# Optimization experiments

Hardware: AMD Instinct MI355X
Metric: run time of the kernel (lower is better)

The kernel has to match this reference:

```python
import jax, jax.numpy as jnp
import numpy as np

EMBED_DIM = 1024
NUM_HEADS = 16
HEAD_DIM = EMBED_DIM // NUM_HEADS


def setup_inputs() -> dict:
    key = jax.random.key(0)
    ks = jax.random.split(key, 5)
    B, N = 4, 2048
    s_in = 1.0 / np.sqrt(EMBED_DIM)
    return {
        "x": jax.random.normal(ks[0], (B, N, EMBED_DIM), dtype=jnp.float32),
        "qkv_w": jax.random.uniform(ks[1], (3 * EMBED_DIM, EMBED_DIM), jnp.float32, -s_in, s_in),
        "qkv_b": jax.random.uniform(ks[2], (3 * EMBED_DIM,), jnp.float32, -s_in, s_in),
        "o_w": jax.random.uniform(ks[3], (EMBED_DIM, EMBED_DIM), jnp.float32, -s_in, s_in),
        "o_b": jax.random.uniform(ks[4], (EMBED_DIM,), jnp.float32, -s_in, s_in),
    }


def reference(x, qkv_w, qkv_b, o_w, o_b):
    B, N, E = x.shape
    H, D = NUM_HEADS, HEAD_DIM
    # qkv: [B, N, 3E] -> [B, N, H, 3D] -> [B, H, N, 3D], then chunk last dim
    qkv = (jnp.einsum('bne,fe->bnf', x, qkv_w) + qkv_b)
    qkv = qkv.reshape(B, N, H, 3 * D).transpose(0, 2, 1, 3)
    q, k, v = jnp.split(qkv, 3, axis=-1)
    scale = 1.0 / np.sqrt(D)
    scores = jnp.einsum('bhqd,bhkd->bhqk', q, k) * scale
    attn = jax.nn.softmax(scores, axis=-1)  # dropout is identity in eval mode
    out = jnp.einsum('bhqk,bhkd->bhqd', attn, v)
    out = out.transpose(0, 2, 1, 3).reshape(B, N, E)
    return jnp.einsum('bne,fe->bnf', out, o_w) + o_b
```

## Files before the change

kernel.cpp:

```cpp
#include <hip/hip_runtime.h>

typedef unsigned short u16;
typedef float f32x4 __attribute__((ext_vector_type(4)));
typedef float f32x16 __attribute__((ext_vector_type(16)));
typedef short bf16x8 __attribute__((ext_vector_type(8)));
typedef int i32x2 __attribute__((ext_vector_type(2)));

__device__ __forceinline__ u16 f2bf(float f){
  union { float f; unsigned u; } x; x.f = f;
  unsigned r = (x.u + 0x7FFFu + ((x.u >> 16) & 1u)) >> 16;
  return (u16)r;
}

__device__ __forceinline__ unsigned cvtpk(float lo, float hi){
  unsigned r;
  asm("v_cvt_pk_bf16_f32 %0, %1, %2" : "=v"(r) : "v"(lo), "v"(hi));
  return r;
}

__device__ __forceinline__ f32x4 mfma_bf16(bf16x8 a, bf16x8 b, f32x4 c){
  return __builtin_amdgcn_mfma_f32_16x16x32_bf16(a, b, c, 0, 0, 0);
}

__device__ __forceinline__ f32x16 mfma32(bf16x8 a, bf16x8 b, f32x16 c){
  return __builtin_amdgcn_mfma_f32_32x32x16_bf16(a, b, c, 0, 0, 0);
}

__device__ __forceinline__ void gload16(const u16* g, u16* l){
  __builtin_amdgcn_global_load_lds((__attribute__((address_space(1))) void*)g,
                                   (__attribute__((address_space(3))) void*)l, 16, 0, 0);
}

__global__ void cvt_bf16(const float* __restrict__ in, u16* __restrict__ out, int n4){
  int stride = gridDim.x * blockDim.x;
  for (int i = blockIdx.x*blockDim.x + threadIdx.x; i < n4; i += stride){
    float4 v = ((const float4*)in)[i];
    ushort4 o;
    o.x = f2bf(v.x); o.y = f2bf(v.y); o.z = f2bf(v.z); o.w = f2bf(v.w);
    ((ushort4*)out)[i] = o;
  }
}

__device__ __forceinline__ void stage128x32(const u16* src, int ld, u16* lds, int tid){
  int wave = tid >> 6, lane = tid & 63;
#pragma unroll
  for (int i = 0; i < 2; i++){
    int chunk = i*256 + wave*64 + lane;
    int row = chunk >> 2, slot = chunk & 3;
    int col = ((slot ^ (row & 3)) << 3);
    gload16(src + (size_t)row*ld + col, lds + ((size_t)(i*256 + wave*64) << 3));
  }
}

template<int MODE>
__launch_bounds__(256)
__global__ void gemm_bt(const u16* __restrict__ A, const u16* __restrict__ Bw,
                        const float* __restrict__ bias,
                        u16* __restrict__ Qp, u16* __restrict__ Kp, u16* __restrict__ Vt,
                        float* __restrict__ Co, int M, int Nf, int K)
{
  __shared__ u16 lsA[2][128*32];
  __shared__ u16 lsB[2][128*32];
  int tid = threadIdx.x;
  int wave = tid >> 6, lane = tid & 63, grp = lane >> 4, l16 = lane & 15;
  int ntn = Nf >> 7;
  int bm = blockIdx.x / ntn, bn = blockIdx.x % ntn;
  const u16* Ab = A + (size_t)bm*128*K;
  const u16* Bb = Bw + (size_t)bn*128*K;
  int wm = wave >> 1, wn = wave & 1;
  f32x4 acc[4][4] = {};

  stage128x32(Ab, K, lsA[0], tid);
  stage128x32(Bb, K, lsB[0], tid);
  int nk = K >> 5;
  for (int t = 0; t < nk; t++){
    __syncthreads();
    int cur = t & 1;
    if (t + 1 < nk){
      stage128x32(Ab + ((t+1) << 5), K, lsA[cur^1], tid);
      stage128x32(Bb + ((t+1) << 5), K, lsB[cur^1], tid);
    }
    const u16* la = lsA[cur];
    const u16* lb = lsB[cur];
    bf16x8 af[4], bfr[4];
#pragma unroll
    for (int mf = 0; mf < 4; mf++){
      int row = wm*64 + mf*16 + l16;
      af[mf] = *(const bf16x8*)(la + row*32 + ((grp ^ (row & 3)) << 3));
    }
#pragma unroll
    for (int nf = 0; nf < 4; nf++){
      int row = wn*64 + nf*16 + l16;
      bfr[nf] = *(const bf16x8*)(lb + row*32 + ((grp ^ (row & 3)) << 3));
    }
#pragma unroll
    for (int mf = 0; mf < 4; mf++)
#pragma unroll
      for (int nf = 0; nf < 4; nf++)
        acc[mf][nf] = mfma_bf16(af[mf], bfr[nf], acc[mf][nf]);
  }

  int mrow0 = bm*128 + wm*64;
  int f0 = bn*128 + wn*64;
#pragma unroll
  for (int nf = 0; nf < 4; nf++){
    int f = f0 + nf*16 + l16;
    float bv = bias[f];
    if constexpr (MODE == 0){
      int h = f / 192, c = f % 192;
#pragma unroll
      for (int mf = 0; mf < 4; mf++){
        int mbase = mrow0 + mf*16 + grp*4;
        int bb = mbase >> 11, n0 = mbase & 2047;
        size_t bh = (size_t)bb*16 + h;
        if (c >= 128){
          ushort4 w;
          w.x = f2bf(acc[mf][nf][0] + bv);
          w.y = f2bf(acc[mf][nf][1] + bv);
          w.z = f2bf(acc[mf][nf][2] + bv);
          w.w = f2bf(acc[mf][nf][3] + bv);
          *(ushort4*)(Vt + (bh*64 + (size_t)(c - 128))*2048 + n0) = w;
        } else {
          u16* dst = (c < 64) ? Qp : Kp;
          float sc = (c < 64) ? 0.18033688011f : 1.0f;
          int cc = c & 63;
#pragma unroll
          for (int r = 0; r < 4; r++)
            dst[(bh*2048 + n0 + r)*64 + cc] = f2bf((acc[mf][nf][r] + bv) * sc);
        }
      }
    } else {
#pragma unroll
      for (int mf = 0; mf < 4; mf++){
        int mbase = mrow0 + mf*16 + grp*4;
#pragma unroll
        for (int r = 0; r < 4; r++)
          Co[(size_t)(mbase + r)*Nf + f] = acc[mf][nf][r] + bv;
      }
    }
  }
}

__device__ __forceinline__ void stage64x64(const u16* src, int ld, u16* lds, int tid){
  int wave = tid >> 6, lane = tid & 63;
#pragma unroll
  for (int i = 0; i < 2; i++){
    int chunk = i*256 + wave*64 + lane;
    int row = chunk >> 3, slot = chunk & 7;
    int col = ((slot ^ (row & 7)) << 3);
    gload16(src + (size_t)row*ld + col, lds + ((size_t)(i*256 + wave*64) << 3));
  }
}

__launch_bounds__(256, 4)
__global__ void attn_fwd(const u16* __restrict__ Qg, const u16* __restrict__ Kg,
                         const u16* __restrict__ Vtg, u16* __restrict__ Oa)
{
  __shared__ u16 kl[2][64*64];
  __shared__ u16 vl[2][64*64];
  int tid = threadIdx.x;
  int lane = tid & 63, wave = tid >> 6;
  int q32 = lane & 31, hi = lane >> 5;
  int bid = (blockIdx.x & 7) * 128 + (blockIdx.x >> 3);
  int bh = bid >> 4, qt = bid & 15;
  int b = bh >> 4, h = bh & 15;
  int q0 = qt*128 + wave*32;
  const u16* Qb = Qg + ((size_t)bh*2048 + q0)*64;
  const u16* Kb = Kg + (size_t)bh*2048*64;
  const u16* Vb = Vtg + (size_t)bh*64*2048;

  bf16x8 qf[4];
#pragma unroll
  for (int s = 0; s < 4; s++)
    qf[s] = *(const bf16x8*)(Qb + q32*64 + s*16 + hi*8);

  f32x16 lacc = {};
  f32x16 oacc[2] = {};

  stage64x64(Kb, 64, kl[0], tid);
  stage64x64(Vb, 2048, vl[0], tid);

  for (int kt = 0; kt < 32; kt++){
    __syncthreads();
    int cur = kt & 1;
    if (kt + 1 < 32){
      stage64x64(Kb + (size_t)(kt+1)*64*64, 64, kl[cur^1], tid);
      stage64x64(Vb + (kt+1)*64, 2048, vl[cur^1], tid);
    }
    const u16* lk = kl[cur];
    const u16* lv = vl[cur];

    f32x16 p0 = {}, p1 = {};
    __builtin_amdgcn_s_setprio(1);
#pragma unroll
    for (int s = 0; s < 4; s++){
      int r0 = q32;
      bf16x8 k0 = *(const bf16x8*)(lk + r0*64 + (((s*2+hi) ^ (r0 & 7)) << 3));
      p0 = mfma32(k0, qf[s], p0);
      int r1 = 32 + q32;
      bf16x8 k1 = *(const bf16x8*)(lk + r1*64 + (((s*2+hi) ^ (r1 & 7)) << 3));
      p1 = mfma32(k1, qf[s], p1);
    }
    __builtin_amdgcn_s_setprio(0);

#pragma unroll
    for (int r = 0; r < 16; r++) p0[r] = exp2f(p0[r]);
#pragma unroll
    for (int r = 0; r < 16; r++) p1[r] = exp2f(p1[r]);
#pragma unroll
    for (int r = 0; r < 16; r++) lacc[r] += p0[r];
#pragma unroll
    for (int r = 0; r < 16; r++) lacc[r] += p1[r];

#pragma unroll
    for (int ks = 0; ks < 4; ks++){
      const f32x16& pp = (ks < 2) ? p0 : p1;
      int base = (ks & 1) * 8;
      unsigned t0 = cvtpk(pp[base+0], pp[base+1]);
      unsigned t1 = cvtpk(pp[base+2], pp[base+3]);
      unsigned t2 = cvtpk(pp[base+4], pp[base+5]);
      unsigned t3 = cvtpk(pp[base+6], pp[base+7]);
      i32x2 r02 = __builtin_amdgcn_permlane32_swap((int)t0, (int)t2, false, false);
      i32x2 r13 = __builtin_amdgcn_permlane32_swap((int)t1, (int)t3, false, false);
      union { unsigned u[4]; bf16x8 v; } pu;
      pu.u[0] = (unsigned)r02.x;
      pu.u[1] = (unsigned)r13.x;
      pu.u[2] = (unsigned)r02.y;
      pu.u[3] = (unsigned)r13.y;

      __builtin_amdgcn_s_setprio(1);
      int rowd0 = q32;
      bf16x8 v0 = *(const bf16x8*)(lv + rowd0*64 + (((ks*2+hi) ^ (rowd0 & 7)) << 3));
      oacc[0] = mfma32(v0, pu.v, oacc[0]);
      int rowd1 = 32 + q32;
      bf16x8 v1 = *(const bf16x8*)(lv + rowd1*64 + (((ks*2+hi) ^ (rowd1 & 7)) << 3));
      oacc[1] = mfma32(v1, pu.v, oacc[1]);
      __builtin_amdgcn_s_setprio(0);
    }
  }

#pragma unroll
  for (int r = 0; r < 8; r++) lacc[r] += lacc[r+8];
#pragma unroll
  for (int r = 0; r < 4; r++) lacc[r] += lacc[r+4];
  float l = (lacc[0] + lacc[1]) + (lacc[2] + lacc[3]);
  l += __shfl_xor(l, 32, 64);
  float inv = 1.0f / l;

  size_t obase = ((size_t)b*2048 + q0 + q32)*1024 + h*64;
#pragma unroll
  for (int dblk = 0; dblk < 2; dblk++)
#pragma unroll
    for (int rb = 0; rb < 4; rb++){
      ushort4 w;
      w.x = f2bf(oacc[dblk][rb*4+0] * inv);
      w.y = f2bf(oacc[dblk][rb*4+1] * inv);
      w.z = f2bf(oacc[dblk][rb*4+2] * inv);
      w.w = f2bf(oacc[dblk][rb*4+3] * inv);
      *(ushort4*)(Oa + obase + dblk*32 + rb*8 + hi*4) = w;
    }
}

extern "C" void kernel_launch(void* const* d_in, const int* in_sizes, int n_in,
                              void* d_out, int out_size, void* d_ws, size_t ws_size,
                              hipStream_t stream)
{
  const float* x    = (const float*)d_in[0];
  const float* qkvw = (const float*)d_in[1];
  const float* qkvb = (const float*)d_in[2];
  const float* ow   = (const float*)d_in[3];
  const float* ob   = (const float*)d_in[4];
  float* out = (float*)d_out;

  u16* xb = (u16*)d_ws;
  u16* wq = xb + (size_t)8192*1024;
  u16* wo = wq + (size_t)3072*1024;
  u16* Qp = wo + (size_t)1024*1024;
  u16* Kp = Qp + (size_t)64*2048*64;
  u16* Vt = Kp + (size_t)64*2048*64;
  u16* Oa = Vt + (size_t)64*2048*64;

  cvt_bf16<<<1024, 256, 0, stream>>>(x, xb, (8192*1024)/4);
  cvt_bf16<<<512, 256, 0, stream>>>(qkvw, wq, (3072*1024)/4);
  cvt_bf16<<<256, 256, 0, stream>>>(ow, wo, (1024*1024)/4);

  gemm_bt<0><<<64*24, 256, 0, stream>>>(xb, wq, qkvb, Qp, Kp, Vt, nullptr, 8192, 3072, 1024);
  attn_fwd<<<1024, 256, 0, stream>>>(Qp, Kp, Vt, Oa);
  gemm_bt<1><<<64*8, 256, 0, stream>>>(Oa, wo, ob, nullptr, nullptr, nullptr, out, 8192, 1024, 1024);
}
```

Measured before the change: 219.7 us.

## Enlarge QKV GEMM and attention blocks to 512 threads, use raw v_exp_f32

The QKV GEMM now uses 256x128 tiles with 8 waves, so each staged B tile is shared across more rows. The attention kernel processes 256 queries per block with 8 waves, so each K/V tile loaded into LDS is reused by twice as many waves. The exp2f calls are replaced with inline v_exp_f32 asm in groups of four, dropping the library's range handling. The larger blocks cut global K/V and weight traffic per output, at the cost of fewer blocks, and the raw exp loses special-case handling for inputs like denormals.

```diff
diff --git a/kernel.cpp b/kernel.cpp
--- a/kernel.cpp
+++ b/kernel.cpp
@@ -16,6 +16,15 @@
   unsigned r;
   asm("v_cvt_pk_bf16_f32 %0, %1, %2" : "=v"(r) : "v"(lo), "v"(hi));
   return r;
+}
+
+__device__ __forceinline__ void exp4q(float& a, float& b, float& c, float& d){
+  asm("v_exp_f32 %0, %0\n\t"
+      "v_exp_f32 %1, %1\n\t"
+      "v_exp_f32 %2, %2\n\t"
+      "v_exp_f32 %3, %3\n\t"
+      "s_nop 1"
+      : "+v"(a), "+v"(b), "+v"(c), "+v"(d));
 }
 
 __device__ __forceinline__ f32x4 mfma_bf16(bf16x8 a, bf16x8 b, f32x4 c){
@@ -41,44 +50,57 @@
   }
 }
 
-__device__ __forceinline__ void stage128x32(const u16* src, int ld, u16* lds, int tid){
-  int wave = tid >> 6, lane = tid & 63;
-#pragma unroll
-  for (int i = 0; i < 2; i++){
-    int chunk = i*256 + wave*64 + lane;
-    int row = chunk >> 2, slot = chunk & 3;
+template<int NCH, int NTHR>
+__device__ __forceinline__ void stage32(const u16* src, int ld, u16* lds, int tid){
+#pragma unroll
+  for (int i = 0; i < NCH/NTHR; i++){
+    int c = i*NTHR + tid;
+    int row = c >> 2, slot = c & 3;
     int col = ((slot ^ (row & 3)) << 3);
-    gload16(src + (size_t)row*ld + col, lds + ((size_t)(i*256 + wave*64) << 3));
-  }
-}
-
-template<int MODE>
-__launch_bounds__(256)
+    gload16(src + (size_t)row*ld + col, lds + ((size_t)(c & ~63) << 3));
+  }
+}
+
+template<int NTHR>
+__device__ __forceinline__ void stage64(const u16* src, int ld, u16* lds, int tid){
+#pragma unroll
+  for (int i = 0; i < 512/NTHR; i++){
+    int c = i*NTHR + tid;
+    int row = c >> 3, slot = c & 7;
+    int col = ((slot ^ (row & 7)) << 3);
+    gload16(src + (size_t)row*ld + col, lds + ((size_t)(c & ~63) << 3));
+  }
+}
+
+template<int MODE, int WROWS>
+__launch_bounds__(WROWS*128)
 __global__ void gemm_bt(const u16* __restrict__ A, const u16* __restrict__ Bw,
                         const float* __restrict__ bias,
                         u16* __restrict__ Qp, u16* __restrict__ Kp, u16* __restrict__ Vt,
                         float* __restrict__ Co, int M, int Nf, int K)
 {
-  __shared__ u16 lsA[2][128*32];
+  constexpr int BM = WROWS*64;
+  constexpr int NTHR = WROWS*128;
+  __shared__ u16 lsA[2][BM*32];
   __shared__ u16 lsB[2][128*32];
   int tid = threadIdx.x;
   int wave = tid >> 6, lane = tid & 63, grp = lane >> 4, l16 = lane & 15;
   int ntn = Nf >> 7;
   int bm = blockIdx.x / ntn, bn = blockIdx.x % ntn;
-  const u16* Ab = A + (size_t)bm*128*K;
+  const u16* Ab = A + (size_t)bm*BM*K;
   const u16* Bb = Bw + (size_t)bn*128*K;
   int wm = wave >> 1, wn = wave & 1;
   f32x4 acc[4][4] = {};
 
-  stage128x32(Ab, K, lsA[0], tid);
-  stage128x32(Bb, K, lsB[0], tid);
+  stage32<BM*4, NTHR>(Ab, K, lsA[0], tid);
+  stage32<512,  NTHR>(Bb, K, lsB[0], tid);
   int nk = K >> 5;
   for (int t = 0; t < nk; t++){
     __syncthreads();
     int cur = t & 1;
     if (t + 1 < nk){
-      stage128x32(Ab + ((t+1) << 5), K, lsA[cur^1], tid);
-      stage128x32(Bb + ((t+1) << 5), K, lsB[cur^1], tid);
+      stage32<BM*4, NTHR>(Ab + ((t+1) << 5), K, lsA[cur^1], tid);
+      stage32<512,  NTHR>(Bb + ((t+1) << 5), K, lsB[cur^1], tid);
     }
     const u16* la = lsA[cur];
     const u16* lb = lsB[cur];
@@ -100,7 +122,7 @@
         acc[mf][nf] = mfma_bf16(af[mf], bfr[nf], acc[mf][nf]);
   }
 
-  int mrow0 = bm*128 + wm*64;
+  int mrow0 = bm*BM + wm*64;
   int f0 = bn*128 + wn*64;
 #pragma unroll
   for (int nf = 0; nf < 4; nf++){
@@ -141,18 +163,7 @@
   }
 }
 
-__device__ __forceinline__ void stage64x64(const u16* src, int ld, u16* lds, int tid){
-  int wave = tid >> 6, lane = tid & 63;
-#pragma unroll
-  for (int i = 0; i < 2; i++){
-    int chunk = i*256 + wave*64 + lane;
-    int row = chunk >> 3, slot = chunk & 7;
-    int col = ((slot ^ (row & 7)) << 3);
-    gload16(src + (size_t)row*ld + col, lds + ((size_t)(i*256 + wave*64) << 3));
-  }
-}
-
-__launch_bounds__(256, 4)
+__launch_bounds__(512, 4)
 __global__ void attn_fwd(const u16* __restrict__ Qg, const u16* __restrict__ Kg,
                          const u16* __restrict__ Vtg, u16* __restrict__ Oa)
 {
@@ -161,10 +172,10 @@
   int tid = threadIdx.x;
   int lane = tid & 63, wave = tid >> 6;
   int q32 = lane & 31, hi = lane >> 5;
-  int bid = (blockIdx.x & 7) * 128 + (blockIdx.x >> 3);
-  int bh = bid >> 4, qt = bid & 15;
+  int bid = (blockIdx.x & 7) * 64 + (blockIdx.x >> 3);
+  int bh = bid >> 3, qt = bid & 7;
   int b = bh >> 4, h = bh & 15;
-  int q0 = qt*128 + wave*32;
+  int q0 = qt*256 + wave*32;
   const u16* Qb = Qg + ((size_t)bh*2048 + q0)*64;
   const u16* Kb = Kg + (size_t)bh*2048*64;
   const u16* Vb = Vtg + (size_t)bh*64*2048;
@@ -177,15 +188,15 @@
   f32x16 lacc = {};
   f32x16 oacc[2] = {};
 
-  stage64x64(Kb, 64, kl[0], tid);
-  stage64x64(Vb, 2048, vl[0], tid);
+  stage64<512>(Kb, 64, kl[0], tid);
+  stage64<512>(Vb, 2048, vl[0], tid);
 
   for (int kt = 0; kt < 32; kt++){
     __syncthreads();
     int cur = kt & 1;
     if (kt + 1 < 32){
-      stage64x64(Kb + (size_t)(kt+1)*64*64, 64, kl[cur^1], tid);
-      stage64x64(Vb + (kt+1)*64, 2048, vl[cur^1], tid);
+      stage64<512>(Kb + (size_t)(kt+1)*64*64, 64, kl[cur^1], tid);
+      stage64<512>(Vb + (kt+1)*64, 2048, vl[cur^1], tid);
     }
     const u16* lk = kl[cur];
     const u16* lv = vl[cur];
@@ -204,9 +215,17 @@
     __builtin_amdgcn_s_setprio(0);
 
 #pragma unroll
-    for (int r = 0; r < 16; r++) p0[r] = exp2f(p0[r]);
-#pragma unroll
-    for (int r = 0; r < 16; r++) p1[r] = exp2f(p1[r]);
+    for (int r = 0; r < 16; r += 4){
+      float a = p0[r], bq = p0[r+1], cq = p0[r+2], d = p0[r+3];
+      exp4q(a, bq, cq, d);
+      p0[r] = a; p0[r+1] = bq; p0[r+2] = cq; p0[r+3] = d;
+    }
+#pragma unroll
+    for (int r = 0; r < 16; r += 4){
+      float a = p1[r], bq = p1[r+1], cq = p1[r+2], d = p1[r+3];
+      exp4q(a, bq, cq, d);
+      p1[r] = a; p1[r+1] = bq; p1[r+2] = cq; p1[r+3] = d;
+    }
 #pragma unroll
     for (int r = 0; r < 16; r++) lacc[r] += p0[r];
 #pragma unroll
@@ -284,7 +303,7 @@
   cvt_bf16<<<512, 256, 0, stream>>>(qkvw, wq, (3072*1024)/4);
   cvt_bf16<<<256, 256, 0, stream>>>(ow, wo, (1024*1024)/4);
 
-  gemm_bt<0><<<64*24, 256, 0, stream>>>(xb, wq, qkvb, Qp, Kp, Vt, nullptr, 8192, 3072, 1024);
-  attn_fwd<<<1024, 256, 0, stream>>>(Qp, Kp, Vt, Oa);
-  gemm_bt<1><<<64*8, 256, 0, stream>>>(Oa, wo, ob, nullptr, nullptr, nullptr, out, 8192, 1024, 1024);
-}
+  gemm_bt<0,4><<<32*24, 512, 0, stream>>>(xb, wq, qkvb, Qp, Kp, Vt, nullptr, 8192, 3072, 1024);
+  attn_fwd<<<512, 512, 0, stream>>>(Qp, Kp, Vt, Oa);
+  gemm_bt<1,2><<<64*8, 256, 0, stream>>>(Oa, wo, ob, nullptr, nullptr, nullptr, out, 8192, 1024, 1024);
+}
```

Result: faster. 198.1 us (-9.8%).
